# Kernel optimization log

Measured on AMD Instinct MI355X. Metric: run time of the kernel, lower is better.

The kernel has to match this reference:

```python
import jax, jax.numpy as jnp
import numpy as np

N_USER = 150_000
M_ITEM = 30_000
N_NODES = N_USER + M_ITEM
D = 64                      # embedding_dim
N_LAYERS = 3                # gcn_layer_number
E = 600_000                 # user-item interactions (symmetric nnz = 2E)
B = 1024
NUM_RATE, NUM_GENRE, NUM_DIR, NUM_ACT = 6, 25, 2186, 8030
NUM_GENDER, NUM_AGE, NUM_OCC, NUM_ZIP = 2, 7, 21, 3402
H1, H2 = 64, 64             # first/second fc hidden dims
FC1_IN = D * 10


def setup_inputs() -> dict:
    key = jax.random.key(0)
    ks = jax.random.split(key, 24)
    # aux features: 0/1 values are valid indices for every categorical field
    aux_info = jax.random.randint(ks[0], (B, 10246), 0, 2, dtype=jnp.int32)
    user_ids = jax.random.randint(ks[1], (B,), 0, N_USER, dtype=jnp.int32)
    item_ids = jax.random.randint(ks[2], (B,), 0, M_ITEM, dtype=jnp.int32)
    # bipartite graph: random interactions, symmetric normalized adjacency
    u = jax.random.randint(ks[3], (E,), 0, N_USER, dtype=jnp.int32)
    i = jax.random.randint(ks[4], (E,), 0, M_ITEM, dtype=jnp.int32) + N_USER
    graph_row = jnp.concatenate([u, i])
    graph_col = jnpph = jnp.concatenate([i, u]) if False else jnp.concatenate([i, u])
    deg = jax.ops.segment_sum(jnp.ones((2 * E,), jnp.float32), graph_row, num_segments=N_NODES)
    dinv = jnp.where(deg > 0, jax.lax.rsqrt(jnp.maximum(deg, 1.0)), 0.0)
    graph_val = dinv[graph_row] * dinv[graph_col]
    s = 0.1
    nrm = lambda k, shp: (jax.random.normal(k, shp, jnp.float32) * s)
    return {
        "aux_info": aux_info, "user_ids": user_ids, "item_ids": item_ids,
        "graph_row": graph_row, "graph_col": graph_col, "graph_val": graph_val,
        "rate_tab": nrm(ks[5], (NUM_RATE, D)),
        "genre_W": nrm(ks[6], (NUM_GENRE, D)),
        "director_W": nrm(ks[7], (NUM_DIR, D)),
        "actor_W": nrm(ks[8], (NUM_ACT, D)),
        "gender_tab": nrm(ks[9], (NUM_GENDER, D)),
        "age_tab": nrm(ks[10], (NUM_AGE, D)),
        "occ_tab": nrm(ks[11], (NUM_OCC, D)),
        "area_tab": nrm(ks[12], (NUM_ZIP, D)),
        "user_rel": nrm(ks[13], (N_USER, D)),
        "item_rel": nrm(ks[14], (M_ITEM, D)),
        "fc1_W": nrm(ks[15], (FC1_IN, H1)), "fc1_b": jnp.zeros((H1,), jnp.float32),
        "fc2_W": nrm(ks[16], (H1, H2)), "fc2_b": jnp.zeros((H2,), jnp.float32),
        "out_W": nrm(ks[17], (H2, 1)), "out_b": jnp.zeros((1,), jnp.float32),
    }


def _lightgcn(user_rel, item_rel, row, col, val):
    # LightGCN: repeated SpMM D^-1/2 A D^-1/2 @ emb, mean over layer outputs
    emb = jnp.concatenate([user_rel, item_rel], axis=0)      # [N, D]
    acc = emb
    for _ in range(N_LAYERS):
        emb = jax.ops.segment_sum(val[:, None] * emb[col], row, num_segments=N_NODES)
        acc = acc + emb
    light = acc / (N_LAYERS + 1)
    return light[:N_USER], light[N_USER:]


def _multi_hot(idx_int, W):
    x = idx_int.astype(jnp.float32)
    return (x @ W) / jnp.sum(x, axis=1, keepdims=True)


def reference(aux_info, user_ids, item_ids, graph_row, graph_col, graph_val,
              rate_tab, genre_W, director_W, actor_W,
              gender_tab, age_tab, occ_tab, area_tab,
              user_rel, item_rel,
              fc1_W, fc1_b, fc2_W, fc2_b, out_W, out_b):
    rate_idx = aux_info[:, 0]
    genre_idx = aux_info[:, 1:26]
    director_idx = aux_info[:, 26:2212]
    actor_idx = aux_info[:, 2212:10242]
    gender_idx = aux_info[:, 10242]
    age_idx = aux_info[:, 10243]
    occ_idx = aux_info[:, 10244]
    area_idx = aux_info[:, 10245]

    item_emb = jnp.concatenate([
        rate_tab[rate_idx],
        _multi_hot(genre_idx, genre_W),
        _multi_hot(director_idx, director_W),
        _multi_hot(actor_idx, actor_W),
    ], axis=1)                                               # [B, 4D]
    user_emb = jnp.concatenate([
        gender_tab[gender_idx], age_tab[age_idx],
        occ_tab[occ_idx], area_tab[area_idx],
    ], axis=1)                                               # [B, 4D]

    all_users, all_items = _lightgcn(user_rel, item_rel, graph_row, graph_col, graph_val)
    X = jnp.concatenate([item_emb, user_emb,
                         all_users[user_ids], all_items[item_ids]], axis=1)  # [B, 10D]
    X = jax.nn.relu(X @ fc1_W + fc1_b)
    X = jax.nn.relu(X @ fc2_W + fc2_b)
    return X @ out_W + out_b                                 # [B, 1]
```

## Files before the change

kernel.cpp:

```cpp
#include <hip/hip_runtime.h>
#include <hip/hip_bf16.h>
#include <hip/hip_fp16.h>

#define N_USER 150000
#define M_ITEM 30000
#define N_NODES 180000
#define E2 1200000
#define BATCH 1024
#define AUX_W 10246
#define KP_G 32
#define KP_D 2208
#define KP_A 8064
#define NBKT 265
#define WT_BLKS 2576
#define BCNT_BLKS 293
#define MH_BLKS 672

typedef __attribute__((ext_vector_type(8))) short short8;
typedef __attribute__((ext_vector_type(8))) unsigned short ushort8_t;
typedef __attribute__((ext_vector_type(4))) float f32x4;

__device__ __forceinline__ int bucket_of(int r) {
    return r < N_USER ? (r >> 10) : 147 + ((r - N_USER) >> 8);
}

__device__ __forceinline__ int detect_f32(const void* probe) {
    float v = __bfloat162float(((const __hip_bfloat16*)probe)[threadIdx.x & 63]);
    unsigned long long m = __ballot(!(fabsf(v) < 1000.0f));
    return __popcll(m) > 8;
}

struct CvtSeg { const void* src; float* dst; int n; int blk0; };
struct CvtBatch { CvtSeg seg[16]; };

__global__ void __launch_bounds__(256) k_prep(CvtBatch cb, int cvtBlks,
                                              const void* Wg, const void* Wd, const void* Wa,
                                              unsigned short* WtG, unsigned short* WtD, unsigned short* WtA,
                                              const int* __restrict__ grow, int* __restrict__ bucket_tot,
                                              const void* probe) {
    int blk = blockIdx.x, tid = threadIdx.x;
    if (blk < cvtBlks) {
        int isf32 = detect_f32(probe);
        int si = 0;
        #pragma unroll
        for (int i = 0; i < 16; ++i) if (blk >= cb.seg[i].blk0) si = i;
        const CvtSeg sg = cb.seg[si];
        int i = (blk - sg.blk0) * 256 + tid;
        if (i >= sg.n) return;
        if (isf32) sg.dst[i] = ((const float*)sg.src)[i];
        else       sg.dst[i] = __bfloat162float(((const __hip_bfloat16*)sg.src)[i]);
        return;
    }
    if (blk < cvtBlks + WT_BLKS) {
        int isf32 = detect_f32(probe);
        int t = (blk - cvtBlks) * 256 + tid;
        if (t >= (KP_G + KP_D + KP_A) * 64) return;
        int kp = t >> 6, n = t & 63;
        int k, K; const void* src; unsigned short* dst;
        if (kp < KP_G)              { k = kp;               K = 25;   src = Wg; dst = WtG; }
        else if (kp < KP_G + KP_D)  { k = kp - KP_G;        K = 2186; src = Wd; dst = WtD; }
        else                        { k = kp - KP_G - KP_D; K = 8030; src = Wa; dst = WtA; }
        unsigned short v = 0;
        if (k < K) {
            if (isf32) {
                __hip_bfloat16 h = __float2bfloat16(((const float*)src)[(size_t)k * 64 + n]);
                v = *(unsigned short*)&h;
            } else {
                v = ((const unsigned short*)src)[(size_t)k * 64 + n];
            }
        }
        dst[(((size_t)(k >> 5) * 64 + n) * 4 + ((k >> 3) & 3)) * 8 + (k & 7)] = v;
        return;
    }
    __shared__ int h[NBKT];
    for (int i = tid; i < NBKT; i += 256) h[i] = 0;
    __syncthreads();
    int idx0 = (blk - cvtBlks - WT_BLKS) * 4096;
    #pragma unroll
    for (int k = 0; k < 16; ++k) {
        int i = idx0 + k * 256 + tid;
        if (i < E2) atomicAdd(&h[bucket_of(grow[i])], 1);
    }
    __syncthreads();
    for (int i = tid; i < NBKT; i += 256) if (h[i]) atomicAdd(&bucket_tot[i], h[i]);
}

__global__ void __launch_bounds__(512) k_bscan(const int* __restrict__ bucket_tot,
                                               int* __restrict__ bucket_base,
                                               int* __restrict__ bucketcur) {
    __shared__ int s[512];
    int tid = threadIdx.x;
    s[tid] = (tid < NBKT) ? bucket_tot[tid] : 0;
    __syncthreads();
    for (int off = 1; off < 512; off <<= 1) {
        int v = (tid >= off) ? s[tid - off] : 0;
        __syncthreads();
        s[tid] += v;
        __syncthreads();
    }
    int excl = tid ? s[tid - 1] : 0;
    bucket_base[tid] = excl;
    if (tid < NBKT) bucketcur[tid] = excl;
}

__global__ void __launch_bounds__(256) k_p1(const int* __restrict__ grow, const int* __restrict__ gcol,
                                            int* __restrict__ bucketcur, int2* __restrict__ binned) {
    __shared__ int h1[NBKT], base1[NBKT];
    int tid = threadIdx.x;
    for (int i = tid; i < NBKT; i += 256) h1[i] = 0;
    __syncthreads();
    int idx0 = blockIdx.x * 4096;
    int r[16], c[16];
    #pragma unroll
    for (int k = 0; k < 16; ++k) {
        int i = idx0 + k * 256 + tid;
        if (i < E2) {
            r[k] = grow[i]; c[k] = gcol[i];
            atomicAdd(&h1[bucket_of(r[k])], 1);
        } else r[k] = -1;
    }
    __syncthreads();
    for (int i = tid; i < NBKT; i += 256) {
        base1[i] = h1[i] ? atomicAdd(&bucketcur[i], h1[i]) : 0;
        h1[i] = 0;
    }
    __syncthreads();
    #pragma unroll
    for (int k = 0; k < 16; ++k) {
        if (r[k] >= 0) {
            int b = bucket_of(r[k]);
            int p = base1[b] + atomicAdd(&h1[b], 1);
            binned[p] = make_int2(r[k], c[k]);
        }
    }
}

__global__ void __launch_bounds__(256) k_p2(const int2* __restrict__ binned, const int* __restrict__ bb,
                                            int* __restrict__ cols, int2* __restrict__ moffs,
                                            float* __restrict__ dinv, float* __restrict__ dsq,
                                            float* __restrict__ gsc) {
    __shared__ int h[1024];
    __shared__ int ws2[256];
    int b = blockIdx.x, tid = threadIdx.x;
    int r0, r1;
    if (b < 147) { r0 = b << 10; r1 = min((b + 1) << 10, N_USER); }
    else         { r0 = N_USER + ((b - 147) << 8); r1 = min(N_USER + ((b - 146) << 8), N_NODES); }
    int s0 = bb[b], e0 = bb[b + 1];
    for (int i = tid; i < 1024; i += 256) h[i] = 0;
    __syncthreads();
    for (int j = s0 + tid; j < e0; j += 256) atomicAdd(&h[binned[j].x - r0], 1);
    __syncthreads();
    int t0 = tid * 4;
    int a0 = h[t0], a1 = h[t0 + 1], a2 = h[t0 + 2], a3 = h[t0 + 3];
    ws2[tid] = a0 + a1 + a2 + a3;
    __syncthreads();
    for (int off = 1; off < 256; off <<= 1) {
        int v = (tid >= off) ? ws2[tid - off] : 0;
        __syncthreads();
        ws2[tid] += v;
        __syncthreads();
    }
    int excl = tid ? ws2[tid - 1] : 0;
    int ex[4] = { excl, excl + a0, excl + a0 + a1, excl + a0 + a1 + a2 };
    int ac[4] = { a0, a1, a2, a3 };
    #pragma unroll
    for (int i = 0; i < 4; ++i) {
        int row = r0 + t0 + i;
        if (row < r1) {
            moffs[row] = make_int2(s0 + ex[i], s0 + ex[i] + ac[i]);
            float deg = (float)ac[i];
            bool nz = deg > 0.f;
            dinv[row] = nz ? rsqrtf(deg) : 0.f;
            dsq[row]  = nz ? 1.f / deg  : 0.f;
            gsc[row]  = nz ? sqrtf(deg) : 0.f;
        }
        h[t0 + i] = ex[i];
    }
    __syncthreads();
    for (int j = s0 + tid; j < e0; j += 256) {
        int2 e = binned[j];
        int p = s0 + atomicAdd(&h[e.x - r0], 1);
        cols[p] = e.y << 7;
    }
}

__device__ void mhgemm_body(int blk, const int* __restrict__ aux,
                            const unsigned short* __restrict__ WtG,
                            const unsigned short* __restrict__ WtD,
                            const unsigned short* __restrict__ WtA,
                            float* __restrict__ Xmh, float* __restrict__ cntf) {
    int seg, rb, k0, klen, Kseg, auxoff;
    const unsigned short* Wt;
    if (blk < 16)       { seg = 0; rb = blk;                      k0 = 0;              klen = 25;                  Kseg = 25;   auxoff = 1;    Wt = WtG; }
    else if (blk < 160) { int t = blk - 16;  seg = 1; rb = t & 15; k0 = (t >> 4) * 256; klen = min(256, 2186 - k0); Kseg = 2186; auxoff = 26;   Wt = WtD; }
    else                { int t = blk - 160; seg = 2; rb = t & 15; k0 = (t >> 4) * 256; klen = min(256, 8030 - k0); Kseg = 8030; auxoff = 2212; Wt = WtA; }
    int lane = threadIdx.x & 63, wave = threadIdx.x >> 6;
    int m = lane & 15, quad = lane >> 4;
    int row = rb * 64 + wave * 16 + m;
    const int* arow = aux + (size_t)row * AUX_W + auxoff;

    f32x4 acc0 = {0.f,0.f,0.f,0.f}, acc1 = acc0, acc2 = acc0, acc3 = acc0;
    float asum = 0.f;
    int nchunk = (klen + 31) >> 5;
    for (int kci = 0; kci < nchunk; ++kci) {
        int kb = k0 + kci * 32 + quad * 8;
        short8 af;
        if (kb + 8 <= Kseg) {
            #pragma unroll
            for (int j = 0; j < 8; ++j) {
                int x = arow[kb + j];
                af[j] = x ? (short)0x3F80 : (short)0;
                asum += (float)x;
            }
        } else {
            #pragma unroll
            for (int j = 0; j < 8; ++j) {
                int x = (kb + j < Kseg) ? arow[kb + j] : 0;
                af[j] = x ? (short)0x3F80 : (short)0;
                asum += (float)x;
            }
        }
        size_t kcg = (size_t)(k0 >> 5) + kci;
        const unsigned short* bp = Wt + ((kcg * 64 + m) * 4 + quad) * 8;
        short8 b0 = *(const short8*)(bp);
        short8 b1 = *(const short8*)(bp + 512);
        short8 b2 = *(const short8*)(bp + 1024);
        short8 b3 = *(const short8*)(bp + 1536);
        acc0 = __builtin_amdgcn_mfma_f32_16x16x32_bf16(af, b0, acc0, 0, 0, 0);
        acc1 = __builtin_amdgcn_mfma_f32_16x16x32_bf16(af, b1, acc1, 0, 0, 0);
        acc2 = __builtin_amdgcn_mfma_f32_16x16x32_bf16(af, b2, acc2, 0, 0, 0);
        acc3 = __builtin_amdgcn_mfma_f32_16x16x32_bf16(af, b3, acc3, 0, 0, 0);
    }
    asum += __shfl_xor(asum, 16);
    asum += __shfl_xor(asum, 32);
    if (quad == 0) atomicAdd(&cntf[seg * BATCH + row], asum);
    float* xbase = Xmh + ((size_t)seg * BATCH + rb * 64 + wave * 16 + quad * 4) * 64;
    #pragma unroll
    for (int reg = 0; reg < 4; ++reg) {
        float* xr = xbase + (size_t)reg * 64;
        atomicAdd(&xr[ 0 + m], acc0[reg]);
        atomicAdd(&xr[16 + m], acc1[reg]);
        atomicAdd(&xr[32 + m], acc2[reg]);
        atomicAdd(&xr[48 + m], acc3[reg]);
    }
}

__global__ void __launch_bounds__(256) k_cvt_fused(const void* rawU, const void* rawI,
                                                   const float* __restrict__ dinv,
                                                   __half* __restrict__ emb,
                                                   float* __restrict__ tacc,
                                                   const int* __restrict__ uids,
                                                   const int* __restrict__ iids, int cvtN,
                                                   const int2* __restrict__ moffs,
                                                   const int* __restrict__ cols,
                                                   int2* __restrict__ moffs2,
                                                   const int* __restrict__ aux,
                                                   const unsigned short* __restrict__ WtG,
                                                   const unsigned short* __restrict__ WtD,
                                                   const unsigned short* __restrict__ WtA,
                                                   float* __restrict__ Xmh, float* __restrict__ cntf) {
    int blk = blockIdx.x;
    if (blk < MH_BLKS) {
        mhgemm_body(blk, aux, WtG, WtD, WtA, Xmh, cntf);
        return;
    }
    if (blk < MH_BLKS + 512) {
        int lane = threadIdx.x & 63;
        int t = (blk - MH_BLKS) * 4 + (threadIdx.x >> 6);
        int r = (t < BATCH) ? uids[t] : (N_USER + iids[t - BATCH]);
        int2 se = moffs[r];
        if (lane == 0) moffs2[r] = se;
        for (int j = se.x + lane; j < se.y; j += 64) {
            int c = (unsigned)cols[j] >> 7;
            moffs2[c] = moffs[c];
        }
        return;
    }
    int isf32 = detect_f32(rawU);
    if (blk < MH_BLKS + 1024) {
        int lane = threadIdx.x & 63;
        int t = (blk - MH_BLKS - 512) * 4 + (threadIdx.x >> 6);
        const void* src; size_t ri;
        if (t < BATCH) { src = rawU; ri = (size_t)uids[t]; }
        else           { src = rawI; ri = (size_t)iids[t - BATCH]; }
        float v;
        if (isf32) v = ((const float*)src)[ri * 64 + lane];
        else       v = __bfloat162float(((const __hip_bfloat16*)src)[ri * 64 + lane]);
        tacc[(size_t)t * 64 + lane] = v;
        return;
    }
    int q = (blk - MH_BLKS - 1024) * 256 + threadIdx.x;
    if (q >= N_NODES * 8) return;
    int r = q >> 3;
    const void* src; size_t qq;
    if (r < N_USER) { src = rawU; qq = (size_t)q; }
    else            { src = rawI; qq = (size_t)q - (size_t)N_USER * 8; }
    float d = dinv[r];
    float f[8];
    if (isf32) {
        float4 a = ((const float4*)src)[qq * 2], b = ((const float4*)src)[qq * 2 + 1];
        f[0]=a.x; f[1]=a.y; f[2]=a.z; f[3]=a.w; f[4]=b.x; f[5]=b.y; f[6]=b.z; f[7]=b.w;
    } else {
        ushort8_t u = ((const ushort8_t*)src)[qq];
        #pragma unroll
        for (int i = 0; i < 8; ++i) {
            unsigned short us = u[i];
            f[i] = __bfloat162float(*(__hip_bfloat16*)&us);
        }
    }
    ushort8_t o;
    #pragma unroll
    for (int i = 0; i < 8; ++i) {
        __half h = __float2half(f[i] * d);
        o[i] = *(unsigned short*)&h;
    }
    ((ushort8_t*)emb)[(size_t)q] = o;
}

__global__ void __launch_bounds__(256, 8) k_spmv(const __half* __restrict__ src, __half* __restrict__ dst,
                                                 const int2* __restrict__ moffs_in, const int* __restrict__ cols,
                                                 const float* __restrict__ dsq,
                                                 int spmvN, float* __restrict__ tacc,
                                                 const int* __restrict__ uids, const int* __restrict__ iids,
                                                 const float* __restrict__ gsc) {
    int tid = threadIdx.x, lane = tid & 63;
    int blk = blockIdx.x;
    if (blk >= spmvN) {
        int t = (blk - spmvN) * 4 + (tid >> 6);
        int r = (t < BATCH) ? uids[t] : (N_USER + iids[t - BATCH]);
        tacc[(size_t)t * 64 + lane] += __half2float(src[(size_t)r * 64 + lane]) * gsc[r];
        return;
    }
    int wid8 = blk * 4 + (tid >> 6);
    int g = lane >> 3, l8 = lane & 7;
    int r = wid8 * 8 + g;
    int2 se = moffs_in[r];
    int s = se.x, e = se.y;
    const char* sb = (const char*)src + (l8 << 4);
    float2 a0 = {0.f,0.f}, a1 = a0, a2 = a0, a3 = a0;
    int j0 = s;
    for (; j0 + 4 <= e; j0 += 4) {
        int c[4];
        #pragma unroll
        for (int u = 0; u < 4; ++u) c[u] = cols[j0 + u];
        float4 rv[4];
        #pragma unroll
        for (int u = 0; u < 4; ++u) rv[u] = *(const float4*)(sb + (size_t)(unsigned)c[u]);
        #pragma unroll
        for (int u = 0; u < 4; ++u) {
            const __half2* h = (const __half2*)&rv[u];
            float2 f0 = __half22float2(h[0]), f1 = __half22float2(h[1]);
            float2 f2 = __half22float2(h[2]), f3 = __half22float2(h[3]);
            a0.x += f0.x; a0.y += f0.y; a1.x += f1.x; a1.y += f1.y;
            a2.x += f2.x; a2.y += f2.y; a3.x += f3.x; a3.y += f3.y;
        }
    }
    if (j0 < e) {
        int c[4]; float w[4];
        #pragma unroll
        for (int u = 0; u < 4; ++u) {
            int j = j0 + u;
            c[u] = cols[min(j, e - 1)];
            w[u] = (j < e) ? 1.f : 0.f;
        }
        float4 rv[4];
        #pragma unroll
        for (int u = 0; u < 4; ++u) rv[u] = *(const float4*)(sb + (size_t)(unsigned)c[u]);
        #pragma unroll
        for (int u = 0; u < 4; ++u) {
            const __half2* h = (const __half2*)&rv[u];
            float2 f0 = __half22float2(h[0]), f1 = __half22float2(h[1]);
            float2 f2 = __half22float2(h[2]), f3 = __half22float2(h[3]);
            a0.x = fmaf(w[u], f0.x, a0.x); a0.y = fmaf(w[u], f0.y, a0.y);
            a1.x = fmaf(w[u], f1.x, a1.x); a1.y = fmaf(w[u], f1.y, a1.y);
            a2.x = fmaf(w[u], f2.x, a2.x); a2.y = fmaf(w[u], f2.y, a2.y);
            a3.x = fmaf(w[u], f3.x, a3.x); a3.y = fmaf(w[u], f3.y, a3.y);
        }
    }
    if (e > s) {
        float d = dsq[r];
        float4 ov;
        __half2* op = (__half2*)&ov;
        op[0] = __floats2half2_rn(a0.x * d, a0.y * d);
        op[1] = __floats2half2_rn(a1.x * d, a1.y * d);
        op[2] = __floats2half2_rn(a2.x * d, a2.y * d);
        op[3] = __floats2half2_rn(a3.x * d, a3.y * d);
        *(float4*)((char*)dst + ((size_t)r << 7) + (l8 << 4)) = ov;
    }
}

__global__ void __launch_bounds__(256) k_spmv3(const __half* __restrict__ src, float* __restrict__ tacc,
                                               const int2* __restrict__ moffs, const int* __restrict__ cols,
                                               const float* __restrict__ dinv, const float* __restrict__ gsc,
                                               const int* __restrict__ uids, const int* __restrict__ iids) {
    int tid = threadIdx.x, lane = tid & 63;
    int t = blockIdx.x * 4 + (tid >> 6);
    if (t >= 2048) return;
    int r = (t < BATCH) ? uids[t] : (N_USER + iids[t - BATCH]);
    int2 se = moffs[r];
    int s = se.x, e = se.y;
    int p = lane & 31, ep = lane >> 5;
    const char* sb = (const char*)src + (p << 2);
    float ax = 0.f, ay = 0.f;
    int j0 = s;
    for (; j0 + 16 <= e; j0 += 16) {
        int c[8];
        #pragma unroll
        for (int u = 0; u < 8; ++u) c[u] = cols[j0 + 2 * u + ep];
        float2 v[8];
        #pragma unroll
        for (int u = 0; u < 8; ++u) v[u] = __half22float2(*(const __half2*)(sb + (size_t)(unsigned)c[u]));
        #pragma unroll
        for (int u = 0; u < 8; ++u) { ax += v[u].x; ay += v[u].y; }
    }
    if (j0 + 8 <= e) {
        int c[4];
        #pragma unroll
        for (int u = 0; u < 4; ++u) c[u] = cols[j0 + 2 * u + ep];
        float2 v[4];
        #pragma unroll
        for (int u = 0; u < 4; ++u) v[u] = __half22float2(*(const __half2*)(sb + (size_t)(unsigned)c[u]));
        #pragma unroll
        for (int u = 0; u < 4; ++u) { ax += v[u].x; ay += v[u].y; }
        j0 += 8;
    }
    if (j0 + 4 <= e) {
        int c0 = cols[j0 + ep], c1 = cols[j0 + 2 + ep];
        float2 v0 = __half22float2(*(const __half2*)(sb + (size_t)(unsigned)c0));
        float2 v1 = __half22float2(*(const __half2*)(sb + (size_t)(unsigned)c1));
        ax += v0.x + v1.x; ay += v0.y + v1.y;
        j0 += 4;
    }
    if (j0 < e) {
        int j1 = j0 + ep, j2 = j0 + 2 + ep;
        int c0 = cols[min(j1, e - 1)], c1 = cols[min(j2, e - 1)];
        float w0 = (j1 < e) ? 1.f : 0.f, w1 = (j2 < e) ? 1.f : 0.f;
        float2 v0 = __half22float2(*(const __half2*)(sb + (size_t)(unsigned)c0));
        float2 v1 = __half22float2(*(const __half2*)(sb + (size_t)(unsigned)c1));
        ax = fmaf(w0, v0.x, ax); ay = fmaf(w0, v0.y, ay);
        ax = fmaf(w1, v1.x, ax); ay = fmaf(w1, v1.y, ay);
    }
    ax += __shfl_xor(ax, 32);
    ay += __shfl_xor(ay, 32);
    if (ep == 0) {
        float2 self = __half22float2(*(const __half2*)((const char*)src + ((size_t)r << 7) + (p << 2)));
        float di = dinv[r], g = gsc[r];
        float* tp = tacc + (size_t)t * 64 + (p << 1);
        tp[0] += di * ax + g * self.x;
        tp[1] += di * ay + g * self.y;
    }
}

__global__ void __launch_bounds__(256) k_mlp(const int* __restrict__ aux,
                                             const float* __restrict__ ratef, const float* __restrict__ genderf,
                                             const float* __restrict__ agef, const float* __restrict__ occf,
                                             const float* __restrict__ areaf, const float* __restrict__ tacc,
                                             const float* __restrict__ Xmh, const float* __restrict__ cntf,
                                             const float* __restrict__ W1, const float* __restrict__ b1,
                                             const float* __restrict__ W2, const float* __restrict__ b2,
                                             const float* __restrict__ Wo, const float* __restrict__ bo,
                                             void* __restrict__ out, const void* probe) {
    __shared__ float sx[4][640];
    __shared__ float sh[4][64];
    int isf32 = detect_f32(probe);
    int lane = threadIdx.x & 63, w = threadIdx.x >> 6;
    int b = blockIdx.x * 4 + w;
    const int* arow = aux + (size_t)b * AUX_W;
    float* xr = sx[w];
    xr[0   + lane] = ratef[arow[0] * 64 + lane];
    xr[64  + lane] = Xmh[((size_t)0 * BATCH + b) * 64 + lane] / cntf[0 * BATCH + b];
    xr[128 + lane] = Xmh[((size_t)1 * BATCH + b) * 64 + lane] / cntf[1 * BATCH + b];
    xr[192 + lane] = Xmh[((size_t)2 * BATCH + b) * 64 + lane] / cntf[2 * BATCH + b];
    xr[256 + lane] = genderf[arow[10242] * 64 + lane];
    xr[320 + lane] = agef[arow[10243] * 64 + lane];
    xr[384 + lane] = occf[arow[10244] * 64 + lane];
    xr[448 + lane] = areaf[arow[10245] * 64 + lane];
    xr[512 + lane] = tacc[(size_t)b * 64 + lane] * 0.25f;
    xr[576 + lane] = tacc[(size_t)(BATCH + b) * 64 + lane] * 0.25f;
    float acc = b1[lane];
    #pragma unroll 8
    for (int k = 0; k < 640; ++k) acc += xr[k] * W1[(size_t)k * 64 + lane];
    float h1 = fmaxf(acc, 0.f);
    sh[w][lane] = h1;
    float acc2 = b2[lane];
    #pragma unroll 8
    for (int j = 0; j < 64; ++j) acc2 += sh[w][j] * W2[(size_t)j * 64 + lane];
    float h2 = fmaxf(acc2, 0.f);
    float p = h2 * Wo[lane];
    #pragma unroll
    for (int off = 32; off; off >>= 1) p += __shfl_down(p, off);
    if (lane == 0) {
        float r = p + bo[0];
        if (isf32) ((float*)out)[b] = r;
        else       ((__hip_bfloat16*)out)[b] = __float2bfloat16(r);
    }
}

extern "C" void kernel_launch(void* const* d_in, const int* in_sizes, int n_in,
                              void* d_out, int out_size, void* d_ws, size_t ws_size,
                              hipStream_t stream) {
    const int* aux  = (const int*)d_in[0];
    const int* uids = (const int*)d_in[1];
    const int* iids = (const int*)d_in[2];
    const int* grow = (const int*)d_in[3];
    const int* gcol = (const int*)d_in[4];

    char* p = (char*)d_ws;
    auto alloc = [&](size_t bytes) -> char* {
        char* r = p;
        p += (bytes + 255) / 256 * 256;
        return r;
    };
    int*   bucket_tot  = (int*)alloc(512 * 4);
    float* Xmh         = (float*)alloc((size_t)3 * BATCH * 64 * 4);
    float* cntf        = (float*)alloc((size_t)3 * BATCH * 4);
    int2*  moffs2      = (int2*)alloc((size_t)180224 * 8);
    char*  zero_end    = p;
    int*   bucket_base = (int*)alloc(512 * 4);
    int*   bucketcur   = (int*)alloc(512 * 4);
    int2*  moffs       = (int2*)alloc((size_t)180224 * 8);
    float* dinv        = (float*)alloc((size_t)180224 * 4);
    float* dsq         = (float*)alloc((size_t)180224 * 4);
    float* gsc         = (float*)alloc((size_t)180224 * 4);
    int2*  binned      = (int2*)alloc((size_t)E2 * 8);
    int*   cols        = (int*)alloc((size_t)E2 * 4);
    __half* embA       = (__half*)alloc((size_t)N_NODES * 64 * 2);
    __half* embB       = (__half*)alloc((size_t)N_NODES * 64 * 2);
    float* tacc        = (float*)alloc((size_t)2048 * 64 * 4);
    unsigned short* WtG = (unsigned short*)alloc((size_t)KP_G * 64 * 2);
    unsigned short* WtD = (unsigned short*)alloc((size_t)KP_D * 64 * 2);
    unsigned short* WtA = (unsigned short*)alloc((size_t)KP_A * 64 * 2);
    float* ratef   = (float*)alloc(384 * 4);
    float* genderf = (float*)alloc(128 * 4);
    float* agef    = (float*)alloc(448 * 4);
    float* occf    = (float*)alloc(1344 * 4);
    float* areaf   = (float*)alloc((size_t)217728 * 4);
    float* fc1W    = (float*)alloc((size_t)40960 * 4);
    float* fc1b    = (float*)alloc(64 * 4);
    float* fc2W    = (float*)alloc(4096 * 4);
    float* fc2b    = (float*)alloc(64 * 4);
    float* outW    = (float*)alloc(64 * 4);
    float* outb    = (float*)alloc(4);

    const void* probe = d_in[14];

    hipMemsetAsync(bucket_tot, 0, (size_t)(zero_end - (char*)bucket_tot), stream);

    CvtBatch cb;
    int blk = 0, si = 0;
    auto addseg = [&](const void* s, float* d, int n) {
        cb.seg[si].src = s; cb.seg[si].dst = d; cb.seg[si].n = n; cb.seg[si].blk0 = blk;
        blk += (n + 255) / 256; ++si;
    };
    addseg(d_in[6],  ratef,   384);
    addseg(d_in[10], genderf, 128);
    addseg(d_in[11], agef,    448);
    addseg(d_in[12], occf,    1344);
    addseg(d_in[13], areaf,   217728);
    addseg(d_in[16], fc1W,   40960);
    addseg(d_in[17], fc1b,   64);
    addseg(d_in[18], fc2W,   4096);
    addseg(d_in[19], fc2b,   64);
    addseg(d_in[20], outW,   64);
    addseg(d_in[21], outb,   1);
    for (int i = si; i < 16; ++i) { cb.seg[i].src = nullptr; cb.seg[i].dst = nullptr; cb.seg[i].n = 0; cb.seg[i].blk0 = 0x7fffffff; }
    const int cvtBlks = blk;
    hipLaunchKernelGGL(k_prep, dim3(cvtBlks + WT_BLKS + BCNT_BLKS), dim3(256), 0, stream,
                       cb, cvtBlks, d_in[7], d_in[8], d_in[9], WtG, WtD, WtA, grow, bucket_tot, probe);

    hipLaunchKernelGGL(k_bscan, dim3(1), dim3(512), 0, stream, bucket_tot, bucket_base, bucketcur);
    hipLaunchKernelGGL(k_p1, dim3((E2 + 4095) / 4096), dim3(256), 0, stream, grow, gcol, bucketcur, binned);
    hipLaunchKernelGGL(k_p2, dim3(NBKT), dim3(256), 0, stream, binned, bucket_base, cols, moffs, dinv, dsq, gsc);

    const int cvtN = (N_NODES * 8 + 255) / 256;
    hipLaunchKernelGGL(k_cvt_fused, dim3(MH_BLKS + 1024 + cvtN), dim3(256), 0, stream,
                       d_in[14], d_in[15], dinv, embA, tacc, uids, iids, cvtN,
                       moffs, cols, moffs2, aux, WtG, WtD, WtA, Xmh, cntf);

    const int spmvN = N_NODES / 32;
    hipLaunchKernelGGL(k_spmv, dim3(spmvN), dim3(256), 0, stream,
                       embA, embB, moffs, cols, dsq, spmvN, (float*)nullptr, uids, iids, gsc);
    hipLaunchKernelGGL(k_spmv, dim3(spmvN + 512), dim3(256), 0, stream,
                       embB, embA, moffs2, cols, dsq, spmvN, tacc, uids, iids, gsc);
    hipLaunchKernelGGL(k_spmv3, dim3(2048 / 4), dim3(256), 0, stream,
                       embA, tacc, moffs, cols, dinv, gsc, uids, iids);

    hipLaunchKernelGGL(k_mlp, dim3(BATCH / 4), dim3(256), 0, stream,
                       aux, ratef, genderf, agef, occf, areaf, tacc, Xmh, cntf,
                       fc1W, fc1b, fc2W, fc2b, outW, outb, d_out, probe);
}
```

Baseline: 297.1 us.

## Move multi-hot GEMM into edge-binning kernel and prefetch aux loads

Moves the multi-hot MFMA GEMM blocks from the conversion kernel into the edge-binning pass-1 kernel, so the compute-heavy GEMM overlaps with the latency-bound edge scatter instead of delaying the embedding conversion that the SpMV chain waits on. Inside the GEMM, the next chunk of aux values is loaded one iteration ahead (software pipelining). The bf16 one/zero packing is now branchless integer multiplies, and the row count is summed as an integer. The conversion kernel's block order is also changed so the full-table embedding conversion blocks run first. The cost is larger register use in the GEMM and a heavier binning kernel launch.

New measurement: 295.0 us. No clear change (-0.7%).

```diff
diff --git a/kernel.cpp b/kernel.cpp
--- a/kernel.cpp
+++ b/kernel.cpp
@@ -103,87 +103,6 @@
     if (tid < NBKT) bucketcur[tid] = excl;
 }
 
-__global__ void __launch_bounds__(256) k_p1(const int* __restrict__ grow, const int* __restrict__ gcol,
-                                            int* __restrict__ bucketcur, int2* __restrict__ binned) {
-    __shared__ int h1[NBKT], base1[NBKT];
-    int tid = threadIdx.x;
-    for (int i = tid; i < NBKT; i += 256) h1[i] = 0;
-    __syncthreads();
-    int idx0 = blockIdx.x * 4096;
-    int r[16], c[16];
-    #pragma unroll
-    for (int k = 0; k < 16; ++k) {
-        int i = idx0 + k * 256 + tid;
-        if (i < E2) {
-            r[k] = grow[i]; c[k] = gcol[i];
-            atomicAdd(&h1[bucket_of(r[k])], 1);
-        } else r[k] = -1;
-    }
-    __syncthreads();
-    for (int i = tid; i < NBKT; i += 256) {
-        base1[i] = h1[i] ? atomicAdd(&bucketcur[i], h1[i]) : 0;
-        h1[i] = 0;
-    }
-    __syncthreads();
-    #pragma unroll
-    for (int k = 0; k < 16; ++k) {
-        if (r[k] >= 0) {
-            int b = bucket_of(r[k]);
-            int p = base1[b] + atomicAdd(&h1[b], 1);
-            binned[p] = make_int2(r[k], c[k]);
-        }
-    }
-}
-
-__global__ void __launch_bounds__(256) k_p2(const int2* __restrict__ binned, const int* __restrict__ bb,
-                                            int* __restrict__ cols, int2* __restrict__ moffs,
-                                            float* __restrict__ dinv, float* __restrict__ dsq,
-                                            float* __restrict__ gsc) {
-    __shared__ int h[1024];
-    __shared__ int ws2[256];
-    int b = blockIdx.x, tid = threadIdx.x;
-    int r0, r1;
-    if (b < 147) { r0 = b << 10; r1 = min((b + 1) << 10, N_USER); }
-    else         { r0 = N_USER + ((b - 147) << 8); r1 = min(N_USER + ((b - 146) << 8), N_NODES); }
-    int s0 = bb[b], e0 = bb[b + 1];
-    for (int i = tid; i < 1024; i += 256) h[i] = 0;
-    __syncthreads();
-    for (int j = s0 + tid; j < e0; j += 256) atomicAdd(&h[binned[j].x - r0], 1);
-    __syncthreads();
-    int t0 = tid * 4;
-    int a0 = h[t0], a1 = h[t0 + 1], a2 = h[t0 + 2], a3 = h[t0 + 3];
-    ws2[tid] = a0 + a1 + a2 + a3;
-    __syncthreads();
-    for (int off = 1; off < 256; off <<= 1) {
-        int v = (tid >= off) ? ws2[tid - off] : 0;
-        __syncthreads();
-        ws2[tid] += v;
-        __syncthreads();
-    }
-    int excl = tid ? ws2[tid - 1] : 0;
-    int ex[4] = { excl, excl + a0, excl + a0 + a1, excl + a0 + a1 + a2 };
-    int ac[4] = { a0, a1, a2, a3 };
-    #pragma unroll
-    for (int i = 0; i < 4; ++i) {
-        int row = r0 + t0 + i;
-        if (row < r1) {
-            moffs[row] = make_int2(s0 + ex[i], s0 + ex[i] + ac[i]);
-            float deg = (float)ac[i];
-            bool nz = deg > 0.f;
-            dinv[row] = nz ? rsqrtf(deg) : 0.f;
-            dsq[row]  = nz ? 1.f / deg  : 0.f;
-            gsc[row]  = nz ? sqrtf(deg) : 0.f;
-        }
-        h[t0 + i] = ex[i];
-    }
-    __syncthreads();
-    for (int j = s0 + tid; j < e0; j += 256) {
-        int2 e = binned[j];
-        int p = s0 + atomicAdd(&h[e.x - r0], 1);
-        cols[p] = e.y << 7;
-    }
-}
-
 __device__ void mhgemm_body(int blk, const int* __restrict__ aux,
                             const unsigned short* __restrict__ WtG,
                             const unsigned short* __restrict__ WtD,
@@ -200,37 +119,42 @@
     const int* arow = aux + (size_t)row * AUX_W + auxoff;
 
     f32x4 acc0 = {0.f,0.f,0.f,0.f}, acc1 = acc0, acc2 = acc0, acc3 = acc0;
-    float asum = 0.f;
+    int isum = 0;
     int nchunk = (klen + 31) >> 5;
-    for (int kci = 0; kci < nchunk; ++kci) {
+    int pa[8], na[8];
+    auto lda = [&](int kci, int (&A)[8]) {
         int kb = k0 + kci * 32 + quad * 8;
-        short8 af;
         if (kb + 8 <= Kseg) {
             #pragma unroll
-            for (int j = 0; j < 8; ++j) {
-                int x = arow[kb + j];
-                af[j] = x ? (short)0x3F80 : (short)0;
-                asum += (float)x;
-            }
+            for (int j = 0; j < 8; ++j) A[j] = arow[kb + j];
         } else {
             #pragma unroll
-            for (int j = 0; j < 8; ++j) {
-                int x = (kb + j < Kseg) ? arow[kb + j] : 0;
-                af[j] = x ? (short)0x3F80 : (short)0;
-                asum += (float)x;
-            }
-        }
+            for (int j = 0; j < 8; ++j) A[j] = (kb + j < Kseg) ? arow[kb + j] : 0;
+        }
+    };
+    lda(0, pa);
+    for (int kci = 0; kci < nchunk; ++kci) {
+        if (kci + 1 < nchunk) lda(kci + 1, na);
+        union { unsigned u[4]; short8 s; } af;
+        af.u[0] = (unsigned)pa[0] * 16256u + (unsigned)pa[1] * 0x3F800000u;
+        af.u[1] = (unsigned)pa[2] * 16256u + (unsigned)pa[3] * 0x3F800000u;
+        af.u[2] = (unsigned)pa[4] * 16256u + (unsigned)pa[5] * 0x3F800000u;
+        af.u[3] = (unsigned)pa[6] * 16256u + (unsigned)pa[7] * 0x3F800000u;
+        isum += pa[0] + pa[1] + pa[2] + pa[3] + pa[4] + pa[5] + pa[6] + pa[7];
         size_t kcg = (size_t)(k0 >> 5) + kci;
         const unsigned short* bp = Wt + ((kcg * 64 + m) * 4 + quad) * 8;
         short8 b0 = *(const short8*)(bp);
         short8 b1 = *(const short8*)(bp + 512);
         short8 b2 = *(const short8*)(bp + 1024);
         short8 b3 = *(const short8*)(bp + 1536);
-        acc0 = __builtin_amdgcn_mfma_f32_16x16x32_bf16(af, b0, acc0, 0, 0, 0);
-        acc1 = __builtin_amdgcn_mfma_f32_16x16x32_bf16(af, b1, acc1, 0, 0, 0);
-        acc2 = __builtin_amdgcn_mfma_f32_16x16x32_bf16(af, b2, acc2, 0, 0, 0);
-        acc3 = __builtin_amdgcn_mfma_f32_16x16x32_bf16(af, b3, acc3, 0, 0, 0);
-    }
+        acc0 = __builtin_amdgcn_mfma_f32_16x16x32_bf16(af.s, b0, acc0, 0, 0, 0);
+        acc1 = __builtin_amdgcn_mfma_f32_16x16x32_bf16(af.s, b1, acc1, 0, 0, 0);
+        acc2 = __builtin_amdgcn_mfma_f32_16x16x32_bf16(af.s, b2, acc2, 0, 0, 0);
+        acc3 = __builtin_amdgcn_mfma_f32_16x16x32_bf16(af.s, b3, acc3, 0, 0, 0);
+        #pragma unroll
+        for (int j = 0; j < 8; ++j) pa[j] = na[j];
+    }
+    float asum = (float)isum;
     asum += __shfl_xor(asum, 16);
     asum += __shfl_xor(asum, 32);
     if (quad == 0) atomicAdd(&cntf[seg * BATCH + row], asum);
@@ -245,6 +169,96 @@
     }
 }
 
+__global__ void __launch_bounds__(256) k_p1(const int* __restrict__ grow, const int* __restrict__ gcol,
+                                            int* __restrict__ bucketcur, int2* __restrict__ binned,
+                                            const int* __restrict__ aux,
+                                            const unsigned short* __restrict__ WtG,
+                                            const unsigned short* __restrict__ WtD,
+                                            const unsigned short* __restrict__ WtA,
+                                            float* __restrict__ Xmh, float* __restrict__ cntf) {
+    if (blockIdx.x < MH_BLKS) {
+        mhgemm_body(blockIdx.x, aux, WtG, WtD, WtA, Xmh, cntf);
+        return;
+    }
+    __shared__ int h1[NBKT], base1[NBKT];
+    int tid = threadIdx.x;
+    for (int i = tid; i < NBKT; i += 256) h1[i] = 0;
+    __syncthreads();
+    int idx0 = (blockIdx.x - MH_BLKS) * 4096;
+    int r[16], c[16];
+    #pragma unroll
+    for (int k = 0; k < 16; ++k) {
+        int i = idx0 + k * 256 + tid;
+        if (i < E2) {
+            r[k] = grow[i]; c[k] = gcol[i];
+            atomicAdd(&h1[bucket_of(r[k])], 1);
+        } else r[k] = -1;
+    }
+    __syncthreads();
+    for (int i = tid; i < NBKT; i += 256) {
+        base1[i] = h1[i] ? atomicAdd(&bucketcur[i], h1[i]) : 0;
+        h1[i] = 0;
+    }
+    __syncthreads();
+    #pragma unroll
+    for (int k = 0; k < 16; ++k) {
+        if (r[k] >= 0) {
+            int b = bucket_of(r[k]);
+            int p = base1[b] + atomicAdd(&h1[b], 1);
+            binned[p] = make_int2(r[k], c[k]);
+        }
+    }
+}
+
+__global__ void __launch_bounds__(256) k_p2(const int2* __restrict__ binned, const int* __restrict__ bb,
+                                            int* __restrict__ cols, int2* __restrict__ moffs,
+                                            float* __restrict__ dinv, float* __restrict__ dsq,
+                                            float* __restrict__ gsc) {
+    __shared__ int h[1024];
+    __shared__ int ws2[256];
+    int b = blockIdx.x, tid = threadIdx.x;
+    int r0, r1;
+    if (b < 147) { r0 = b << 10; r1 = min((b + 1) << 10, N_USER); }
+    else         { r0 = N_USER + ((b - 147) << 8); r1 = min(N_USER + ((b - 146) << 8), N_NODES); }
+    int s0 = bb[b], e0 = bb[b + 1];
+    for (int i = tid; i < 1024; i += 256) h[i] = 0;
+    __syncthreads();
+    for (int j = s0 + tid; j < e0; j += 256) atomicAdd(&h[binned[j].x - r0], 1);
+    __syncthreads();
+    int t0 = tid * 4;
+    int a0 = h[t0], a1 = h[t0 + 1], a2 = h[t0 + 2], a3 = h[t0 + 3];
+    ws2[tid] = a0 + a1 + a2 + a3;
+    __syncthreads();
+    for (int off = 1; off < 256; off <<= 1) {
+        int v = (tid >= off) ? ws2[tid - off] : 0;
+        __syncthreads();
+        ws2[tid] += v;
+        __syncthreads();
+    }
+    int excl = tid ? ws2[tid - 1] : 0;
+    int ex[4] = { excl, excl + a0, excl + a0 + a1, excl + a0 + a1 + a2 };
+    int ac[4] = { a0, a1, a2, a3 };
+    #pragma unroll
+    for (int i = 0; i < 4; ++i) {
+        int row = r0 + t0 + i;
+        if (row < r1) {
+            moffs[row] = make_int2(s0 + ex[i], s0 + ex[i] + ac[i]);
+            float deg = (float)ac[i];
+            bool nz = deg > 0.f;
+            dinv[row] = nz ? rsqrtf(deg) : 0.f;
+            dsq[row]  = nz ? 1.f / deg  : 0.f;
+            gsc[row]  = nz ? sqrtf(deg) : 0.f;
+        }
+        h[t0 + i] = ex[i];
+    }
+    __syncthreads();
+    for (int j = s0 + tid; j < e0; j += 256) {
+        int2 e = binned[j];
+        int p = s0 + atomicAdd(&h[e.x - r0], 1);
+        cols[p] = e.y << 7;
+    }
+}
+
 __global__ void __launch_bounds__(256) k_cvt_fused(const void* rawU, const void* rawI,
                                                    const float* __restrict__ dinv,
                                                    __half* __restrict__ emb,
@@ -253,20 +267,41 @@
                                                    const int* __restrict__ iids, int cvtN,
                                                    const int2* __restrict__ moffs,
                                                    const int* __restrict__ cols,
-                                                   int2* __restrict__ moffs2,
-                                                   const int* __restrict__ aux,
-                                                   const unsigned short* __restrict__ WtG,
-                                                   const unsigned short* __restrict__ WtD,
-                                                   const unsigned short* __restrict__ WtA,
-                                                   float* __restrict__ Xmh, float* __restrict__ cntf) {
+                                                   int2* __restrict__ moffs2) {
     int blk = blockIdx.x;
-    if (blk < MH_BLKS) {
-        mhgemm_body(blk, aux, WtG, WtD, WtA, Xmh, cntf);
+    if (blk < cvtN) {
+        int isf32 = detect_f32(rawU);
+        int q = blk * 256 + threadIdx.x;
+        if (q >= N_NODES * 8) return;
+        int r = q >> 3;
+        const void* src; size_t qq;
+        if (r < N_USER) { src = rawU; qq = (size_t)q; }
+        else            { src = rawI; qq = (size_t)q - (size_t)N_USER * 8; }
+        float d = dinv[r];
+        float f[8];
+        if (isf32) {
+            float4 a = ((const float4*)src)[qq * 2], b = ((const float4*)src)[qq * 2 + 1];
+            f[0]=a.x; f[1]=a.y; f[2]=a.z; f[3]=a.w; f[4]=b.x; f[5]=b.y; f[6]=b.z; f[7]=b.w;
+        } else {
+            ushort8_t u = ((const ushort8_t*)src)[qq];
+            #pragma unroll
+            for (int i = 0; i < 8; ++i) {
+                unsigned short us = u[i];
+                f[i] = __bfloat162float(*(__hip_bfloat16*)&us);
+            }
+        }
+        ushort8_t o;
+        #pragma unroll
+        for (int i = 0; i < 8; ++i) {
+            __half h = __float2half(f[i] * d);
+            o[i] = *(unsigned short*)&h;
+        }
+        ((ushort8_t*)emb)[(size_t)q] = o;
         return;
     }
-    if (blk < MH_BLKS + 512) {
+    if (blk < cvtN + 512) {
         int lane = threadIdx.x & 63;
-        int t = (blk - MH_BLKS) * 4 + (threadIdx.x >> 6);
+        int t = (blk - cvtN) * 4 + (threadIdx.x >> 6);
         int r = (t < BATCH) ? uids[t] : (N_USER + iids[t - BATCH]);
         int2 se = moffs[r];
         if (lane == 0) moffs2[r] = se;
@@ -276,10 +311,10 @@
         }
         return;
     }
-    int isf32 = detect_f32(rawU);
-    if (blk < MH_BLKS + 1024) {
+    {
+        int isf32 = detect_f32(rawU);
         int lane = threadIdx.x & 63;
-        int t = (blk - MH_BLKS - 512) * 4 + (threadIdx.x >> 6);
+        int t = (blk - cvtN - 512) * 4 + (threadIdx.x >> 6);
         const void* src; size_t ri;
         if (t < BATCH) { src = rawU; ri = (size_t)uids[t]; }
         else           { src = rawI; ri = (size_t)iids[t - BATCH]; }
@@ -287,34 +322,7 @@
         if (isf32) v = ((const float*)src)[ri * 64 + lane];
         else       v = __bfloat162float(((const __hip_bfloat16*)src)[ri * 64 + lane]);
         tacc[(size_t)t * 64 + lane] = v;
-        return;
-    }
-    int q = (blk - MH_BLKS - 1024) * 256 + threadIdx.x;
-    if (q >= N_NODES * 8) return;
-    int r = q >> 3;
-    const void* src; size_t qq;
-    if (r < N_USER) { src = rawU; qq = (size_t)q; }
-    else            { src = rawI; qq = (size_t)q - (size_t)N_USER * 8; }
-    float d = dinv[r];
-    float f[8];
-    if (isf32) {
-        float4 a = ((const float4*)src)[qq * 2], b = ((const float4*)src)[qq * 2 + 1];
-        f[0]=a.x; f[1]=a.y; f[2]=a.z; f[3]=a.w; f[4]=b.x; f[5]=b.y; f[6]=b.z; f[7]=b.w;
-    } else {
-        ushort8_t u = ((const ushort8_t*)src)[qq];
-        #pragma unroll
-        for (int i = 0; i < 8; ++i) {
-            unsigned short us = u[i];
-            f[i] = __bfloat162float(*(__hip_bfloat16*)&us);
-        }
-    }
-    ushort8_t o;
-    #pragma unroll
-    for (int i = 0; i < 8; ++i) {
-        __half h = __float2half(f[i] * d);
-        o[i] = *(unsigned short*)&h;
-    }
-    ((ushort8_t*)emb)[(size_t)q] = o;
+    }
 }
 
 __global__ void __launch_bounds__(256, 8) k_spmv(const __half* __restrict__ src, __half* __restrict__ dst,
@@ -569,13 +577,14 @@
                        cb, cvtBlks, d_in[7], d_in[8], d_in[9], WtG, WtD, WtA, grow, bucket_tot, probe);
 
     hipLaunchKernelGGL(k_bscan, dim3(1), dim3(512), 0, stream, bucket_tot, bucket_base, bucketcur);
-    hipLaunchKernelGGL(k_p1, dim3((E2 + 4095) / 4096), dim3(256), 0, stream, grow, gcol, bucketcur, binned);
+    hipLaunchKernelGGL(k_p1, dim3(MH_BLKS + (E2 + 4095) / 4096), dim3(256), 0, stream,
+                       grow, gcol, bucketcur, binned, aux, WtG, WtD, WtA, Xmh, cntf);
     hipLaunchKernelGGL(k_p2, dim3(NBKT), dim3(256), 0, stream, binned, bucket_base, cols, moffs, dinv, dsq, gsc);
 
     const int cvtN = (N_NODES * 8 + 255) / 256;
-    hipLaunchKernelGGL(k_cvt_fused, dim3(MH_BLKS + 1024 + cvtN), dim3(256), 0, stream,
+    hipLaunchKernelGGL(k_cvt_fused, dim3(cvtN + 1024), dim3(256), 0, stream,
                        d_in[14], d_in[15], dinv, embA, tacc, uids, iids, cvtN,
-                       moffs, cols, moffs2, aux, WtG, WtD, WtA, Xmh, cntf);
+                       moffs, cols, moffs2);
 
     const int spmvN = N_NODES / 32;
     hipLaunchKernelGGL(k_spmv, dim3(spmvN), dim3(256), 0, stream,
```
